# Performance work log

Hardware: AMD Instinct MI355X
Metric: run time of the kernel (lower is better)

Reference implementation:

```python
import jax, jax.numpy as jnp
import numpy as np

N_NODES = 8192
N_EDGES = 262144
N_VIEWS = 2


def setup_inputs() -> dict:
    key = jax.random.key(0)
    k1, k2, k3, k4, k5, k6 = jax.random.split(key, 6)
    x = jax.random.normal(k1, (N_NODES, 512), dtype=jnp.float32)
    # Glorot-ish scaling for GCN weights
    W1 = jax.random.normal(k2, (512, 256), dtype=jnp.float32) * (1.0 / np.sqrt(512))
    W2 = jax.random.normal(k3, (256, 128), dtype=jnp.float32) * (1.0 / np.sqrt(256))
    edge_vals = jax.random.uniform(k4, (N_EDGES,), dtype=jnp.float32)
    edge_rows = jax.random.randint(k5, (N_EDGES,), 0, N_NODES, dtype=jnp.int32)
    edge_cols = jax.random.randint(k6, (N_EDGES,), 0, N_NODES, dtype=jnp.int32)
    return {"x": x, "W1": W1, "W2": W2, "edge_vals": edge_vals,
            "edge_rows": edge_rows, "edge_cols": edge_cols}


def reference(x, W1, W2, edge_vals, edge_rows, edge_cols):
    # GraphConvolution: support = x @ W ; out = spmm(adj, support) ; act (relu, dropout=0)
    def spmm(h):
        # out[i] = sum_e A[rows[e], cols[e]] * h[cols[e]]  -- irregular gather + segment reduce
        return jax.ops.segment_sum(edge_vals[:, None] * h[edge_cols], edge_rows,
                                   num_segments=N_NODES)

    # Forward quirk in the source: every view uses adjs[0], and mean over n_views
    # identical embeddings == a single pass, so one spmm per layer is exact.
    h = jax.nn.relu(spmm(x @ W1))        # [N, 256]
    z = jax.nn.relu(spmm(h @ W2))        # [N, 128]  (self.embeddings)

    # InnerProductDecoder with act = identity (lambda x: x from Model_2 default)
    rec = z @ z.T                         # [N, N]
    rec_views = jnp.stack([rec] * N_VIEWS, axis=0)  # n_views identical decoders
    return z, rec_views
```

## Files before the change

### kernel.cpp

```cpp
#include <hip/hip_runtime.h>

#define NN 8192
#define NE 262144

typedef short bf16x8 __attribute__((ext_vector_type(8)));
typedef float f32x16 __attribute__((ext_vector_type(16)));

__device__ __forceinline__ unsigned short f2bf(float f) {
  unsigned u = __float_as_uint(f);
  u += 0x7fffu + ((u >> 16) & 1u);
  return (unsigned short)(u >> 16);
}

__global__ void k_prep(const float* __restrict__ W1, const float* __restrict__ W2,
                       unsigned short* __restrict__ W1t, unsigned short* __restrict__ W2t,
                       int* __restrict__ counts) {
  int id = blockIdx.x * blockDim.x + threadIdx.x;
  int stride = gridDim.x * blockDim.x;
  for (int t = id; t < 512 * 256; t += stride) {
    int k = t >> 8, c = t & 255;
    W1t[c * 512 + k] = f2bf(W1[t]);
  }
  for (int t = id; t < 256 * 128; t += stride) {
    int k = t >> 7, c = t & 127;
    W2t[c * 256 + k] = f2bf(W2[t]);
  }
  for (int t = id; t < NN; t += stride) counts[t] = 0;
}

__global__ void k_hist(const int* __restrict__ rows, int* __restrict__ counts) {
  int id = blockIdx.x * blockDim.x + threadIdx.x;
  if (id < NE) atomicAdd(&counts[rows[id]], 1);
}

__global__ void k_scan(const int* __restrict__ counts, int* __restrict__ starts,
                       int* __restrict__ cursor) {
  __shared__ int sums[1024];
  int t = threadIdx.x;
  int base = t * 8;
  int local[8];
  int s = 0;
  #pragma unroll
  for (int i = 0; i < 8; ++i) { local[i] = s; s += counts[base + i]; }
  sums[t] = s;
  __syncthreads();
  for (int off = 1; off < 1024; off <<= 1) {
    int v = 0;
    if (t >= off) v = sums[t - off];
    __syncthreads();
    sums[t] += v;
    __syncthreads();
  }
  int pre = sums[t] - s;
  #pragma unroll
  for (int i = 0; i < 8; ++i) {
    starts[base + i] = pre + local[i];
    cursor[base + i] = pre + local[i];
  }
  if (t == 1023) starts[NN] = sums[1023];
}

__global__ void k_scatter(const int* __restrict__ rows, int* __restrict__ cursor,
                          int* __restrict__ perm) {
  int id = blockIdx.x * blockDim.x + threadIdx.x;
  if (id < NE) {
    int pos = atomicAdd(&cursor[rows[id]], 1);
    perm[pos] = id;
  }
}

template <int K, int N, bool AF32>
__global__ __launch_bounds__(256) void k_gemm(const float* __restrict__ Af,
                                              const unsigned short* __restrict__ Ab,
                                              const unsigned short* __restrict__ Bt,
                                              float* __restrict__ C) {
  __shared__ unsigned char As[128 * 64 * 2];
  __shared__ unsigned char Bs[64 * 64 * 2];
  const int tid = threadIdx.x;
  const int r0 = blockIdx.x * 128, c0 = blockIdx.y * 64;
  const int wid = tid >> 6, lane = tid & 63;
  const int wrow = wid >> 1, wcol = wid & 1;
  const int lr = lane & 31, lg = lane >> 5;

  f32x16 acc[2] = {};

  for (int kc = 0; kc < K; kc += 64) {
    __syncthreads();
    if constexpr (AF32) {
      for (int q = tid; q < 1024; q += 256) {
        int r = q >> 3, s = q & 7;
        const float* gp = Af + (size_t)(r0 + r) * K + kc + s * 8;
        float4 v0 = *(const float4*)gp;
        float4 v1 = *(const float4*)(gp + 4);
        unsigned lo0 = (unsigned)f2bf(v0.x) | ((unsigned)f2bf(v0.y) << 16);
        unsigned hi0 = (unsigned)f2bf(v0.z) | ((unsigned)f2bf(v0.w) << 16);
        unsigned lo1 = (unsigned)f2bf(v1.x) | ((unsigned)f2bf(v1.y) << 16);
        unsigned hi1 = (unsigned)f2bf(v1.z) | ((unsigned)f2bf(v1.w) << 16);
        uint4 u = make_uint4(lo0, hi0, lo1, hi1);
        *(uint4*)(As + r * 128 + ((s * 16) ^ ((r & 7) << 4))) = u;
      }
    } else {
      for (int q = tid; q < 1024; q += 256) {
        int r = q >> 3, s = q & 7;
        float4 v = *(const float4*)(Ab + (size_t)(r0 + r) * K + kc + s * 8);
        *(float4*)(As + r * 128 + ((s * 16) ^ ((r & 7) << 4))) = v;
      }
    }
    for (int q = tid; q < 512; q += 256) {
      int r = q >> 3, s = q & 7;
      float4 v = *(const float4*)(Bt + (size_t)(c0 + r) * K + kc + s * 8);
      *(float4*)(Bs + r * 128 + ((s * 16) ^ ((r & 7) << 4))) = v;
    }
    __syncthreads();
    #pragma unroll
    for (int ks = 0; ks < 4; ++ks) {
      int brow = wcol * 32 + lr;
      bf16x8 bf = *(const bf16x8*)(Bs + brow * 128 + ((ks * 32 + lg * 16) ^ ((brow & 7) << 4)));
      #pragma unroll
      for (int m = 0; m < 2; ++m) {
        int arow = wrow * 64 + m * 32 + lr;
        bf16x8 af = *(const bf16x8*)(As + arow * 128 + ((ks * 32 + lg * 16) ^ ((arow & 7) << 4)));
        acc[m] = __builtin_amdgcn_mfma_f32_32x32x16_bf16(af, bf, acc[m], 0, 0, 0);
      }
    }
  }
  #pragma unroll
  for (int m = 0; m < 2; ++m) {
    #pragma unroll
    for (int r = 0; r < 16; ++r) {
      int row = r0 + wrow * 64 + m * 32 + (r & 3) + 8 * (r >> 2) + 4 * lg;
      int col = c0 + wcol * 32 + lr;
      C[(size_t)row * N + col] = acc[m][r];
    }
  }
}

template <int F>
__global__ __launch_bounds__(256) void k_spmm(const int* __restrict__ starts,
                                              const int* __restrict__ perm,
                                              const float* __restrict__ vals,
                                              const int* __restrict__ cols,
                                              const float* __restrict__ S,
                                              float* __restrict__ outF,
                                              unsigned short* __restrict__ outB) {
  constexpr int V = F / 64;
  int gw = (blockIdx.x * blockDim.x + threadIdx.x) >> 6;
  int lane = threadIdx.x & 63;
  if (gw >= NN) return;
  int s = starts[gw], e = starts[gw + 1];
  float acc[V];
  #pragma unroll
  for (int v = 0; v < V; ++v) acc[v] = 0.f;
  for (int j = s; j < e; ++j) {
    int eid = perm[j];
    float w = vals[eid];
    const float* p = S + (size_t)cols[eid] * F + lane * V;
    if constexpr (V == 4) {
      float4 t = *(const float4*)p;
      acc[0] += w * t.x; acc[1] += w * t.y; acc[2] += w * t.z; acc[3] += w * t.w;
    } else {
      float2 t = *(const float2*)p;
      acc[0] += w * t.x; acc[1] += w * t.y;
    }
  }
  #pragma unroll
  for (int v = 0; v < V; ++v) acc[v] = fmaxf(acc[v], 0.f);
  if constexpr (V == 4) {
    unsigned lo = (unsigned)f2bf(acc[0]) | ((unsigned)f2bf(acc[1]) << 16);
    unsigned hi = (unsigned)f2bf(acc[2]) | ((unsigned)f2bf(acc[3]) << 16);
    *(uint2*)(outB + (size_t)gw * F + lane * 4) = make_uint2(lo, hi);
  } else {
    unsigned lo = (unsigned)f2bf(acc[0]) | ((unsigned)f2bf(acc[1]) << 16);
    *(unsigned int*)(outB + (size_t)gw * F + lane * 2) = lo;
    if (outF) {
      *(float2*)(outF + (size_t)gw * F + lane * 2) = make_float2(acc[0], acc[1]);
    }
  }
}

__global__ __launch_bounds__(256) void k_rec(const unsigned short* __restrict__ zb,
                                             float* __restrict__ out0,
                                             float* __restrict__ out1) {
  __shared__ unsigned char As[128 * 128 * 2];
  __shared__ unsigned char Bs[64 * 128 * 2];
  const int tid = threadIdx.x;
  const int i0 = blockIdx.x * 128, j0 = blockIdx.y * 64;

  for (int q = tid; q < 2048; q += 256) {
    int r = q >> 4, s = q & 15;
    float4 v = *(const float4*)(zb + (size_t)(i0 + r) * 128 + s * 8);
    *(float4*)(As + r * 256 + ((s * 16) ^ ((r & 15) << 4))) = v;
  }
  for (int q = tid; q < 1024; q += 256) {
    int r = q >> 4, s = q & 15;
    float4 v = *(const float4*)(zb + (size_t)(j0 + r) * 128 + s * 8);
    *(float4*)(Bs + r * 256 + ((s * 16) ^ ((r & 15) << 4))) = v;
  }
  __syncthreads();

  const int wid = tid >> 6, lane = tid & 63;
  const int wrow = wid >> 1, wcol = wid & 1;
  const int lr = lane & 31, lg = lane >> 5;

  f32x16 acc[2] = {};
  #pragma unroll
  for (int ks = 0; ks < 8; ++ks) {
    int brow = wcol * 32 + lr;
    bf16x8 bf = *(const bf16x8*)(Bs + brow * 256 + ((ks * 32 + lg * 16) ^ ((brow & 15) << 4)));
    #pragma unroll
    for (int m = 0; m < 2; ++m) {
      int arow = wrow * 64 + m * 32 + lr;
      bf16x8 af = *(const bf16x8*)(As + arow * 256 + ((ks * 32 + lg * 16) ^ ((arow & 15) << 4)));
      acc[m] = __builtin_amdgcn_mfma_f32_32x32x16_bf16(af, bf, acc[m], 0, 0, 0);
    }
  }
  #pragma unroll
  for (int m = 0; m < 2; ++m) {
    #pragma unroll
    for (int r = 0; r < 16; ++r) {
      size_t row = i0 + wrow * 64 + m * 32 + (r & 3) + 8 * (r >> 2) + 4 * lg;
      size_t col = j0 + wcol * 32 + lr;
      size_t idx = row * NN + col;
      __builtin_nontemporal_store(acc[m][r], out0 + idx);
      __builtin_nontemporal_store(acc[m][r], out1 + idx);
    }
  }
}

extern "C" void kernel_launch(void* const* d_in, const int* in_sizes, int n_in,
                              void* d_out, int out_size, void* d_ws, size_t ws_size,
                              hipStream_t stream) {
  const float* x     = (const float*)d_in[0];
  const float* W1    = (const float*)d_in[1];
  const float* W2    = (const float*)d_in[2];
  const float* evals = (const float*)d_in[3];
  const int*   erows = (const int*)d_in[4];
  const int*   ecols = (const int*)d_in[5];

  float* out_z   = (float*)d_out;
  float* out_r0  = out_z + (size_t)NN * 128;
  float* out_r1  = out_r0 + (size_t)NN * NN;

  char* w = (char*)d_ws;
  unsigned short* W1t = (unsigned short*)w;  w += 256 * 512 * 2;
  unsigned short* W2t = (unsigned short*)w;  w += 128 * 256 * 2;
  float*          s1  = (float*)w;           w += (size_t)NN * 256 * 4;
  unsigned short* hb  = (unsigned short*)w;  w += (size_t)NN * 256 * 2;
  float*          s2  = (float*)w;           w += (size_t)NN * 128 * 4;
  unsigned short* zb  = (unsigned short*)w;  w += (size_t)NN * 128 * 2;
  int* counts = (int*)w;                     w += NN * 4;
  int* starts = (int*)w;                     w += (NN + 8) * 4;
  int* cursor = (int*)w;                     w += NN * 4;
  int* perm   = (int*)w;                     w += NE * 4;

  k_prep<<<256, 256, 0, stream>>>(W1, W2, W1t, W2t, counts);
  k_hist<<<NE / 256, 256, 0, stream>>>(erows, counts);
  k_scan<<<1, 1024, 0, stream>>>(counts, starts, cursor);
  k_scatter<<<NE / 256, 256, 0, stream>>>(erows, cursor, perm);

  k_gemm<512, 256, true><<<dim3(64, 4), 256, 0, stream>>>(x, nullptr, W1t, s1);
  k_spmm<256><<<NN / 4, 256, 0, stream>>>(starts, perm, evals, ecols, s1, nullptr, hb);
  k_gemm<256, 128, false><<<dim3(64, 2), 256, 0, stream>>>(nullptr, hb, W2t, s2);
  k_spmm<128><<<NN / 4, 256, 0, stream>>>(starts, perm, evals, ecols, s2, out_z, zb);
  k_rec<<<dim3(64, 128), 256, 0, stream>>>(zb, out_r0, out_r1);
}
```

Measured before the change: 733.3 us.

## Use bf16 intermediates, pre-permuted edges, and vectorized transposed output stores

Swaps MFMA operand order so each lane holds four consecutive output columns, enabling 16-byte vector stores in the rec and gemm epilogues. GEMM outputs are stored as bf16, so the SpMM gathers read half the bytes. Edge values and columns are scattered into CSR order, removing the perm indirection. x is converted to bf16 in a separate prep pass, which adds an extra read and write, and the bf16 intermediates lower precision.

```diff
diff --git a/kernel.cpp b/kernel.cpp
--- a/kernel.cpp
+++ b/kernel.cpp
@@ -5,18 +5,28 @@
 
 typedef short bf16x8 __attribute__((ext_vector_type(8)));
 typedef float f32x16 __attribute__((ext_vector_type(16)));
+typedef float f32x4 __attribute__((ext_vector_type(4)));
 
 __device__ __forceinline__ unsigned short f2bf(float f) {
   unsigned u = __float_as_uint(f);
   u += 0x7fffu + ((u >> 16) & 1u);
   return (unsigned short)(u >> 16);
 }
-
-__global__ void k_prep(const float* __restrict__ W1, const float* __restrict__ W2,
+__device__ __forceinline__ float bflo(unsigned u) { return __uint_as_float(u << 16); }
+__device__ __forceinline__ float bfhi(unsigned u) { return __uint_as_float(u & 0xffff0000u); }
+
+__global__ void k_prep(const float* __restrict__ x, const float* __restrict__ W1,
+                       const float* __restrict__ W2, unsigned short* __restrict__ xb,
                        unsigned short* __restrict__ W1t, unsigned short* __restrict__ W2t,
                        int* __restrict__ counts) {
   int id = blockIdx.x * blockDim.x + threadIdx.x;
   int stride = gridDim.x * blockDim.x;
+  for (int t = id; t < (NN * 512) / 4; t += stride) {
+    float4 v = *(const float4*)(x + (size_t)t * 4);
+    unsigned lo = (unsigned)f2bf(v.x) | ((unsigned)f2bf(v.y) << 16);
+    unsigned hi = (unsigned)f2bf(v.z) | ((unsigned)f2bf(v.w) << 16);
+    *(uint2*)(xb + (size_t)t * 4) = make_uint2(lo, hi);
+  }
   for (int t = id; t < 512 * 256; t += stride) {
     int k = t >> 8, c = t & 255;
     W1t[c * 512 + k] = f2bf(W1[t]);
@@ -60,20 +70,21 @@
   if (t == 1023) starts[NN] = sums[1023];
 }
 
-__global__ void k_scatter(const int* __restrict__ rows, int* __restrict__ cursor,
-                          int* __restrict__ perm) {
+__global__ void k_scatter(const int* __restrict__ rows, const float* __restrict__ vals,
+                          const int* __restrict__ cols, int* __restrict__ cursor,
+                          float* __restrict__ ev_s, int* __restrict__ ec_s) {
   int id = blockIdx.x * blockDim.x + threadIdx.x;
   if (id < NE) {
     int pos = atomicAdd(&cursor[rows[id]], 1);
-    perm[pos] = id;
-  }
-}
-
-template <int K, int N, bool AF32>
-__global__ __launch_bounds__(256) void k_gemm(const float* __restrict__ Af,
-                                              const unsigned short* __restrict__ Ab,
+    ev_s[pos] = vals[id];
+    ec_s[pos] = cols[id];
+  }
+}
+
+template <int K, int N>
+__global__ __launch_bounds__(256) void k_gemm(const unsigned short* __restrict__ Ab,
                                               const unsigned short* __restrict__ Bt,
-                                              float* __restrict__ C) {
+                                              unsigned short* __restrict__ Cb) {
   __shared__ unsigned char As[128 * 64 * 2];
   __shared__ unsigned char Bs[64 * 64 * 2];
   const int tid = threadIdx.x;
@@ -86,25 +97,10 @@
 
   for (int kc = 0; kc < K; kc += 64) {
     __syncthreads();
-    if constexpr (AF32) {
-      for (int q = tid; q < 1024; q += 256) {
-        int r = q >> 3, s = q & 7;
-        const float* gp = Af + (size_t)(r0 + r) * K + kc + s * 8;
-        float4 v0 = *(const float4*)gp;
-        float4 v1 = *(const float4*)(gp + 4);
-        unsigned lo0 = (unsigned)f2bf(v0.x) | ((unsigned)f2bf(v0.y) << 16);
-        unsigned hi0 = (unsigned)f2bf(v0.z) | ((unsigned)f2bf(v0.w) << 16);
-        unsigned lo1 = (unsigned)f2bf(v1.x) | ((unsigned)f2bf(v1.y) << 16);
-        unsigned hi1 = (unsigned)f2bf(v1.z) | ((unsigned)f2bf(v1.w) << 16);
-        uint4 u = make_uint4(lo0, hi0, lo1, hi1);
-        *(uint4*)(As + r * 128 + ((s * 16) ^ ((r & 7) << 4))) = u;
-      }
-    } else {
-      for (int q = tid; q < 1024; q += 256) {
-        int r = q >> 3, s = q & 7;
-        float4 v = *(const float4*)(Ab + (size_t)(r0 + r) * K + kc + s * 8);
-        *(float4*)(As + r * 128 + ((s * 16) ^ ((r & 7) << 4))) = v;
-      }
+    for (int q = tid; q < 1024; q += 256) {
+      int r = q >> 3, s = q & 7;
+      float4 v = *(const float4*)(Ab + (size_t)(r0 + r) * K + kc + s * 8);
+      *(float4*)(As + r * 128 + ((s * 16) ^ ((r & 7) << 4))) = v;
     }
     for (int q = tid; q < 512; q += 256) {
       int r = q >> 3, s = q & 7;
@@ -120,27 +116,28 @@
       for (int m = 0; m < 2; ++m) {
         int arow = wrow * 64 + m * 32 + lr;
         bf16x8 af = *(const bf16x8*)(As + arow * 128 + ((ks * 32 + lg * 16) ^ ((arow & 7) << 4)));
-        acc[m] = __builtin_amdgcn_mfma_f32_32x32x16_bf16(af, bf, acc[m], 0, 0, 0);
+        acc[m] = __builtin_amdgcn_mfma_f32_32x32x16_bf16(bf, af, acc[m], 0, 0, 0);
       }
     }
   }
   #pragma unroll
   for (int m = 0; m < 2; ++m) {
-    #pragma unroll
-    for (int r = 0; r < 16; ++r) {
-      int row = r0 + wrow * 64 + m * 32 + (r & 3) + 8 * (r >> 2) + 4 * lg;
-      int col = c0 + wcol * 32 + lr;
-      C[(size_t)row * N + col] = acc[m][r];
+    int row = r0 + wrow * 64 + m * 32 + lr;
+    #pragma unroll
+    for (int g = 0; g < 4; ++g) {
+      unsigned lo = (unsigned)f2bf(acc[m][4 * g + 0]) | ((unsigned)f2bf(acc[m][4 * g + 1]) << 16);
+      unsigned hi = (unsigned)f2bf(acc[m][4 * g + 2]) | ((unsigned)f2bf(acc[m][4 * g + 3]) << 16);
+      int colc = c0 + wcol * 32 + 8 * g + 4 * lg;
+      *(uint2*)(Cb + (size_t)row * N + colc) = make_uint2(lo, hi);
     }
   }
 }
 
 template <int F>
 __global__ __launch_bounds__(256) void k_spmm(const int* __restrict__ starts,
-                                              const int* __restrict__ perm,
-                                              const float* __restrict__ vals,
-                                              const int* __restrict__ cols,
-                                              const float* __restrict__ S,
+                                              const float* __restrict__ ev_s,
+                                              const int* __restrict__ ec_s,
+                                              const unsigned short* __restrict__ Sb,
                                               float* __restrict__ outF,
                                               unsigned short* __restrict__ outB) {
   constexpr int V = F / 64;
@@ -152,15 +149,15 @@
   #pragma unroll
   for (int v = 0; v < V; ++v) acc[v] = 0.f;
   for (int j = s; j < e; ++j) {
-    int eid = perm[j];
-    float w = vals[eid];
-    const float* p = S + (size_t)cols[eid] * F + lane * V;
+    float w = ev_s[j];
+    int c = ec_s[j];
     if constexpr (V == 4) {
-      float4 t = *(const float4*)p;
-      acc[0] += w * t.x; acc[1] += w * t.y; acc[2] += w * t.z; acc[3] += w * t.w;
+      uint2 t = *(const uint2*)(Sb + (size_t)c * F + lane * 4);
+      acc[0] += w * bflo(t.x); acc[1] += w * bfhi(t.x);
+      acc[2] += w * bflo(t.y); acc[3] += w * bfhi(t.y);
     } else {
-      float2 t = *(const float2*)p;
-      acc[0] += w * t.x; acc[1] += w * t.y;
+      unsigned t = *(const unsigned*)(Sb + (size_t)c * F + lane * 2);
+      acc[0] += w * bflo(t); acc[1] += w * bfhi(t);
     }
   }
   #pragma unroll
@@ -211,18 +208,18 @@
     for (int m = 0; m < 2; ++m) {
       int arow = wrow * 64 + m * 32 + lr;
       bf16x8 af = *(const bf16x8*)(As + arow * 256 + ((ks * 32 + lg * 16) ^ ((arow & 15) << 4)));
-      acc[m] = __builtin_amdgcn_mfma_f32_32x32x16_bf16(af, bf, acc[m], 0, 0, 0);
+      acc[m] = __builtin_amdgcn_mfma_f32_32x32x16_bf16(bf, af, acc[m], 0, 0, 0);
     }
   }
   #pragma unroll
   for (int m = 0; m < 2; ++m) {
-    #pragma unroll
-    for (int r = 0; r < 16; ++r) {
-      size_t row = i0 + wrow * 64 + m * 32 + (r & 3) + 8 * (r >> 2) + 4 * lg;
-      size_t col = j0 + wcol * 32 + lr;
-      size_t idx = row * NN + col;
-      __builtin_nontemporal_store(acc[m][r], out0 + idx);
-      __builtin_nontemporal_store(acc[m][r], out1 + idx);
+    size_t row = (size_t)(i0 + wrow * 64 + m * 32 + lr);
+    #pragma unroll
+    for (int g = 0; g < 4; ++g) {
+      f32x4 v = {acc[m][4 * g + 0], acc[m][4 * g + 1], acc[m][4 * g + 2], acc[m][4 * g + 3]};
+      size_t idx = row * NN + (size_t)(j0 + wcol * 32 + 8 * g + 4 * lg);
+      __builtin_nontemporal_store(v, (f32x4*)(out0 + idx));
+      __builtin_nontemporal_store(v, (f32x4*)(out1 + idx));
     }
   }
 }
@@ -244,23 +241,25 @@
   char* w = (char*)d_ws;
   unsigned short* W1t = (unsigned short*)w;  w += 256 * 512 * 2;
   unsigned short* W2t = (unsigned short*)w;  w += 128 * 256 * 2;
-  float*          s1  = (float*)w;           w += (size_t)NN * 256 * 4;
-  unsigned short* hb  = (unsigned short*)w;  w += (size_t)NN * 256 * 2;
-  float*          s2  = (float*)w;           w += (size_t)NN * 128 * 4;
+  unsigned short* xb  = (unsigned short*)w;  w += (size_t)NN * 512 * 2;
+  unsigned short* g1  = (unsigned short*)w;  w += (size_t)NN * 256 * 2;
+  unsigned short* h1  = (unsigned short*)w;  w += (size_t)NN * 256 * 2;
+  unsigned short* g2  = (unsigned short*)w;  w += (size_t)NN * 128 * 2;
   unsigned short* zb  = (unsigned short*)w;  w += (size_t)NN * 128 * 2;
-  int* counts = (int*)w;                     w += NN * 4;
-  int* starts = (int*)w;                     w += (NN + 8) * 4;
-  int* cursor = (int*)w;                     w += NN * 4;
-  int* perm   = (int*)w;                     w += NE * 4;
-
-  k_prep<<<256, 256, 0, stream>>>(W1, W2, W1t, W2t, counts);
+  int*   counts = (int*)w;                   w += NN * 4;
+  int*   starts = (int*)w;                   w += (NN + 8) * 4;
+  int*   cursor = (int*)w;                   w += NN * 4;
+  float* ev_s   = (float*)w;                 w += NE * 4;
+  int*   ec_s   = (int*)w;                   w += NE * 4;
+
+  k_prep<<<256, 256, 0, stream>>>(x, W1, W2, xb, W1t, W2t, counts);
   k_hist<<<NE / 256, 256, 0, stream>>>(erows, counts);
   k_scan<<<1, 1024, 0, stream>>>(counts, starts, cursor);
-  k_scatter<<<NE / 256, 256, 0, stream>>>(erows, cursor, perm);
-
-  k_gemm<512, 256, true><<<dim3(64, 4), 256, 0, stream>>>(x, nullptr, W1t, s1);
-  k_spmm<256><<<NN / 4, 256, 0, stream>>>(starts, perm, evals, ecols, s1, nullptr, hb);
-  k_gemm<256, 128, false><<<dim3(64, 2), 256, 0, stream>>>(nullptr, hb, W2t, s2);
-  k_spmm<128><<<NN / 4, 256, 0, stream>>>(starts, perm, evals, ecols, s2, out_z, zb);
+  k_scatter<<<NE / 256, 256, 0, stream>>>(erows, evals, ecols, cursor, ev_s, ec_s);
+
+  k_gemm<512, 256><<<dim3(64, 4), 256, 0, stream>>>(xb, W1t, g1);
+  k_spmm<256><<<NN / 4, 256, 0, stream>>>(starts, ev_s, ec_s, g1, nullptr, h1);
+  k_gemm<256, 128><<<dim3(64, 2), 256, 0, stream>>>(h1, W2t, g2);
+  k_spmm<128><<<NN / 4, 256, 0, stream>>>(starts, ev_s, ec_s, g2, out_z, zb);
   k_rec<<<dim3(64, 128), 256, 0, stream>>>(zb, out_r0, out_r1);
 }
```

Measured after the change: 1.250 ms. 70.4% more time.
